# Kernel optimization log

Hardware: AMD Instinct MI355X
Metric: run time of the kernel (lower is better)

## Reference

```python
import jax, jax.numpy as jnp
import numpy as np

NUM_CLASSES = 128
NUM_DOMAINS = 6
FEAT_DIM = 256
B = 524288
MOMENTUM = 0.9
MARGIN = 1.0


def setup_inputs() -> dict:
    key = jax.random.key(0)
    k1, k2, k3, k4, k5, k6 = jax.random.split(key, 6)
    mu_tilde = jax.random.normal(k1, (B, FEAT_DIM), dtype=jnp.float32)
    anchors = jax.random.normal(k2, (NUM_DOMAINS, NUM_CLASSES, FEAT_DIM), dtype=jnp.float32)
    domain_means = jax.random.normal(k3, (NUM_DOMAINS, FEAT_DIM), dtype=jnp.float32)
    domain_vars = jax.random.uniform(k4, (NUM_DOMAINS, FEAT_DIM), dtype=jnp.float32)
    y_true = jax.random.randint(k5, (B,), 0, NUM_CLASSES, dtype=jnp.int32)
    d_true = jax.random.randint(k6, (B,), 0, NUM_DOMAINS, dtype=jnp.int32)
    return {"mu_tilde": mu_tilde, "anchors": anchors, "domain_means": domain_means,
            "domain_vars": domain_vars, "y_true": y_true, "d_true": d_true}


def reference(mu_tilde, anchors, domain_means, domain_vars, y_true, d_true):
    m = MOMENTUM
    one = jnp.asarray(1.0, mu_tilde.dtype)

    # ---- update(): fused per-(domain,class) segment mean + EMA anchor write ----
    seg = d_true.astype(jnp.int32) * NUM_CLASSES + y_true.astype(jnp.int32)
    n_seg = NUM_DOMAINS * NUM_CLASSES
    seg_sum = jax.ops.segment_sum(mu_tilde, seg, num_segments=n_seg)          # (Nd*C, D)
    seg_cnt = jax.ops.segment_sum(jnp.ones((B,), mu_tilde.dtype), seg, num_segments=n_seg)
    seg_mean = seg_sum / jnp.maximum(seg_cnt, one)[:, None]
    has_samples = (seg_cnt > 0).reshape(NUM_DOMAINS, NUM_CLASSES, 1)
    batch_anchor = seg_mean.reshape(NUM_DOMAINS, NUM_CLASSES, FEAT_DIM)
    new_anchors = jnp.where(has_samples, m * anchors + (1.0 - m) * batch_anchor, anchors)

    # ---- update(): per-domain mean/var (unbiased) + EMA ----
    d_sum = jax.ops.segment_sum(mu_tilde, d_true, num_segments=NUM_DOMAINS)
    d_sq = jax.ops.segment_sum(mu_tilde * mu_tilde, d_true, num_segments=NUM_DOMAINS)
    d_cnt = jax.ops.segment_sum(jnp.ones((B,), mu_tilde.dtype), d_true, num_segments=NUM_DOMAINS)
    safe_cnt = jnp.maximum(d_cnt, one)[:, None]
    b_mean = d_sum / safe_cnt
    b_var = (d_sq - safe_cnt * b_mean * b_mean) / jnp.maximum(d_cnt - 1.0, one)[:, None]
    g = (d_cnt > 1)[:, None]
    new_means = jnp.where(g, m * domain_means + (1.0 - m) * b_mean, domain_means)
    new_vars = jnp.where(g, m * domain_vars + (1.0 - m) * b_var, domain_vars)

    # ---- caa_loss() on updated anchors (all anchors initialized) ----
    class_mean = new_anchors.mean(axis=0, keepdims=True)                      # (1, C, D)
    loss_intra = jnp.mean((new_anchors - class_mean) ** 2)                    # avg of per-class MSE
    A_mean = new_anchors.mean(axis=0)                                         # (C, D)
    sq = jnp.sum(A_mean * A_mean, axis=1)
    d2 = sq[:, None] + sq[None, :] - 2.0 * (A_mean @ A_mean.T)
    off_diag = ~jnp.eye(NUM_CLASSES, dtype=bool)
    d2_safe = jnp.where(off_diag, jnp.maximum(d2, 1e-12), 1.0)
    dist = jnp.sqrt(d2_safe)
    loss_inter = jnp.sum(jnp.where(off_diag, jax.nn.relu(MARGIN - dist), 0.0))
    loss_inter = loss_inter / (NUM_CLASSES * (NUM_CLASSES - 1))
    loss_caa = loss_intra + loss_inter

    # ---- stats_align_loss() on updated stats ----
    global_mean = new_means.mean(axis=0)
    global_var = new_vars.mean(axis=0)
    loss_mean = jnp.mean((new_means - global_mean) ** 2)   # sum_d mse / Nd
    loss_var = jnp.mean((new_vars - global_var) ** 2)
    mu_mean = mu_tilde.mean(axis=0)
    mu_var = jnp.mean(mu_tilde * mu_tilde, axis=0) - mu_mean * mu_mean        # biased var
    loss_mu_mean = jnp.mean((mu_mean - global_mean) ** 2)
    loss_mu_var = jnp.mean((mu_var - global_var) ** 2)
    loss_stats = loss_mean + loss_var + loss_mu_mean + loss_mu_var

    return new_anchors, new_means, new_vars, loss_caa + loss_stats
```

## Files before the change

kernel.cpp:

```cpp
#include <hip/hip_runtime.h>

#define B_N   524288
#define FEAT  256
#define NC    128
#define ND    6
#define NSEG  768
#define CAP   1024

#define ZERO_WORDS 3852

__device__ __forceinline__ float block_reduce(float v, float* lds) {
  #pragma unroll
  for (int o = 32; o > 0; o >>= 1) v += __shfl_down(v, o, 64);
  int wid = threadIdx.x >> 6, lane = threadIdx.x & 63;
  if (lane == 0) lds[wid] = v;
  __syncthreads();
  int nw = (blockDim.x + 63) >> 6;
  v = 0.0f;
  if (wid == 0 && lane < nw) v = lds[lane];
  if (wid == 0) {
    #pragma unroll
    for (int o = 4; o > 0; o >>= 1) v += __shfl_down(v, o, 64);
  }
  return v;
}

#define SCHUNK 4096
#define SCAT_BLOCKS (B_N / SCHUNK)
__global__ __launch_bounds__(1024)
void scatter_k(const int* __restrict__ y, const int* __restrict__ dmn,
               int* __restrict__ cursor, int* __restrict__ slots) {
  __shared__ int lcnt[NSEG];
  __shared__ int lbase[NSEG];
  int t = threadIdx.x;
  if (t < NSEG) lcnt[t] = 0;
  __syncthreads();
  int base = blockIdx.x * SCHUNK;
  int segr[4], lposr[4];
  #pragma unroll
  for (int k = 0; k < 4; ++k) {
    int i = base + t + k * 1024;
    int seg = dmn[i] * NC + y[i];
    segr[k] = seg;
    lposr[k] = atomicAdd(&lcnt[seg], 1);
  }
  __syncthreads();
  if (t < NSEG) lbase[t] = atomicAdd(&cursor[t], lcnt[t]);
  __syncthreads();
  #pragma unroll
  for (int k = 0; k < 4; ++k) {
    int i = base + t + k * 1024;
    int p = lbase[segr[k]] + lposr[k];
    if (p < CAP) slots[segr[k] * CAP + p] = i;
  }
}

__global__ __launch_bounds__(512, 1)
void segreduce_k(const float* __restrict__ mu, const int* __restrict__ slots,
                 const int* __restrict__ cursor, float* __restrict__ seg_sum,
                 float* __restrict__ d_sum_acc, float* __restrict__ d_sq_acc,
                 float* __restrict__ d_cnt) {
  int seg = blockIdx.x;
  int cnt = cursor[seg];
  if (cnt > CAP) cnt = CAP;
  int dom = seg >> 7;
  int t  = threadIdx.x;
  int rr = t >> 6;
  int dq = t & 63;
  const int* sl = slots + seg * CAP;
  const size_t doff = (size_t)(dq << 2);

  float ax=0,ay=0,az=0,aw=0, aqx=0,aqy=0,aqz=0,aqw=0;
  float bx=0,by=0,bz=0,bw=0, bqx=0,bqy=0,bqz=0,bqw=0;

  int r = rr;
  int row0 = (r     < cnt) ? sl[r]     : 0;
  int row1 = (r + 8 < cnt) ? sl[r + 8] : 0;
  while (r + 8 < cnt) {
    int n0 = (r + 16 < cnt) ? sl[r + 16] : 0;
    int n1 = (r + 24 < cnt) ? sl[r + 24] : 0;
    const float4 v0 = *reinterpret_cast<const float4*>(mu + (size_t)row0 * FEAT + doff);
    const float4 v1 = *reinterpret_cast<const float4*>(mu + (size_t)row1 * FEAT + doff);
    ax += v0.x; ay += v0.y; az += v0.z; aw += v0.w;
    aqx += v0.x*v0.x; aqy += v0.y*v0.y; aqz += v0.z*v0.z; aqw += v0.w*v0.w;
    bx += v1.x; by += v1.y; bz += v1.z; bw += v1.w;
    bqx += v1.x*v1.x; bqy += v1.y*v1.y; bqz += v1.z*v1.z; bqw += v1.w*v1.w;
    r += 16; row0 = n0; row1 = n1;
  }
  if (r < cnt) {
    const float4 v0 = *reinterpret_cast<const float4*>(mu + (size_t)row0 * FEAT + doff);
    ax += v0.x; ay += v0.y; az += v0.z; aw += v0.w;
    aqx += v0.x*v0.x; aqy += v0.y*v0.y; aqz += v0.z*v0.z; aqw += v0.w*v0.w;
  }
  ax += bx; ay += by; az += bz; aw += bw;
  aqx += bqx; aqy += bqy; aqz += bqz; aqw += bqw;

  __shared__ float4 redS[512];
  __shared__ float4 redQ[512];
  redS[t] = make_float4(ax, ay, az, aw);
  redQ[t] = make_float4(aqx, aqy, aqz, aqw);
  __syncthreads();
  if (rr == 0) {
    float4 s = redS[t], q = redQ[t];
    #pragma unroll
    for (int g = 1; g < 8; ++g) {
      float4 a = redS[t + 64*g]; s.x+=a.x; s.y+=a.y; s.z+=a.z; s.w+=a.w;
      float4 b = redQ[t + 64*g]; q.x+=b.x; q.y+=b.y; q.z+=b.z; q.w+=b.w;
    }
    *reinterpret_cast<float4*>(seg_sum + (size_t)seg * FEAT + (dq << 2)) = s;
    int base = dom * FEAT + (dq << 2);
    atomicAdd(&d_sum_acc[base+0], s.x); atomicAdd(&d_sum_acc[base+1], s.y);
    atomicAdd(&d_sum_acc[base+2], s.z); atomicAdd(&d_sum_acc[base+3], s.w);
    atomicAdd(&d_sq_acc[base+0], q.x);  atomicAdd(&d_sq_acc[base+1], q.y);
    atomicAdd(&d_sq_acc[base+2], q.z);  atomicAdd(&d_sq_acc[base+3], q.w);
  }
  if (t == 0) atomicAdd(&d_cnt[dom], (float)cnt);
}

__global__ void anchors_k(const float* __restrict__ anchors, const float* __restrict__ seg_sum,
                          const int* __restrict__ cursor, float* __restrict__ out_anchors,
                          float* __restrict__ class_mean, float* __restrict__ sqv,
                          float* __restrict__ loss_acc) {
  int c = blockIdx.x;
  int d = threadIdx.x;
  float na[ND];
  float cm = 0.0f;
  #pragma unroll
  for (int dom = 0; dom < ND; ++dom) {
    int segi = dom * NC + c;
    int cnt = cursor[segi];
    float s = seg_sum[(size_t)segi * FEAT + d];
    float mean = s / fmaxf((float)cnt, 1.0f);
    float a = anchors[(size_t)segi * FEAT + d];
    float v = (cnt > 0) ? (0.9f * a + 0.1f * mean) : a;
    out_anchors[(size_t)segi * FEAT + d] = v;
    na[dom] = v;
    cm += v;
  }
  cm /= 6.0f;
  class_mean[c * FEAT + d] = cm;
  float li = 0.0f;
  #pragma unroll
  for (int dom = 0; dom < ND; ++dom) { float e = na[dom] - cm; li += e * e; }

  __shared__ float rbuf[8];
  float r1 = block_reduce(li, rbuf);
  __syncthreads();
  float r2 = block_reduce(cm * cm, rbuf);
  if (threadIdx.x == 0) { atomicAdd(&loss_acc[0], r1); sqv[c] = r2; }
}

__global__ void inter_k(const float* __restrict__ class_mean, const float* __restrict__ sqv,
                        float* __restrict__ loss_acc) {
  int i = blockIdx.x;
  int j = threadIdx.x;
  __shared__ float Ai[FEAT];
  Ai[j]        = class_mean[i * FEAT + j];
  Ai[j + 128]  = class_mean[i * FEAT + 128 + j];
  __syncthreads();
  const float* Aj = class_mean + (size_t)j * FEAT;
  float dot = 0.0f;
  for (int k = 0; k < FEAT; ++k) dot += Ai[k] * Aj[k];
  float contrib = 0.0f;
  if (i != j) {
    float d2 = sqv[i] + sqv[j] - 2.0f * dot;
    d2 = fmaxf(d2, 1e-12f);
    contrib = fmaxf(1.0f - sqrtf(d2), 0.0f);
  }
  __shared__ float rbuf[8];
  float r = block_reduce(contrib, rbuf);
  if (threadIdx.x == 0) atomicAdd(&loss_acc[1], r);
}

__global__ void stats_k(const float* __restrict__ dmeans, const float* __restrict__ dvars,
                        const float* __restrict__ d_sum_acc, const float* __restrict__ d_sq_acc,
                        const float* __restrict__ d_cnt, float* __restrict__ out_means,
                        float* __restrict__ out_vars, float* __restrict__ loss_acc) {
  int d = threadIdx.x;
  float nm[ND], nv[ND];
  float gm = 0.0f, gv = 0.0f, tsum = 0.0f, tsq = 0.0f;
  #pragma unroll
  for (int dom = 0; dom < ND; ++dom) {
    float cf = d_cnt[dom];
    float safe = fmaxf(cf, 1.0f);
    float su = d_sum_acc[dom * FEAT + d];
    float sq = d_sq_acc[dom * FEAT + d];
    tsum += su; tsq += sq;
    float bm = su / safe;
    float bv = (sq - safe * bm * bm) / fmaxf(cf - 1.0f, 1.0f);
    float m0 = dmeans[dom * FEAT + d], v0 = dvars[dom * FEAT + d];
    bool g = cf > 1.0f;
    float m1 = g ? (0.9f * m0 + 0.1f * bm) : m0;
    float v1 = g ? (0.9f * v0 + 0.1f * bv) : v0;
    out_means[dom * FEAT + d] = m1;
    out_vars[dom * FEAT + d]  = v1;
    nm[dom] = m1; nv[dom] = v1; gm += m1; gv += v1;
  }
  gm /= 6.0f; gv /= 6.0f;
  float lm = 0.0f, lv = 0.0f;
  #pragma unroll
  for (int dom = 0; dom < ND; ++dom) {
    float e = nm[dom] - gm; lm += e * e;
    float f = nv[dom] - gv; lv += f * f;
  }
  float mum = tsum * (1.0f / (float)B_N);
  float muv = tsq * (1.0f / (float)B_N) - mum * mum;
  float lmm = (mum - gm) * (mum - gm);
  float lmv = (muv - gv) * (muv - gv);
  float val = (lm + lv) * (1.0f / 1536.0f) + (lmm + lmv) * (1.0f / 256.0f);
  __shared__ float rbuf[8];
  float r = block_reduce(val, rbuf);
  if (threadIdx.x == 0) loss_acc[2] = r;
}

__global__ void final_k(const float* __restrict__ loss_acc, float* __restrict__ out_loss) {
  *out_loss = loss_acc[0] * (1.0f / 196608.0f)
            + loss_acc[1] * (1.0f / 16256.0f)
            + loss_acc[2];
}

extern "C" void kernel_launch(void* const* d_in, const int* in_sizes, int n_in,
                              void* d_out, int out_size, void* d_ws, size_t ws_size,
                              hipStream_t stream) {
  const float* mu      = (const float*)d_in[0];
  const float* anchors = (const float*)d_in[1];
  const float* dmeans  = (const float*)d_in[2];
  const float* dvars   = (const float*)d_in[3];
  const int*   y       = (const int*)d_in[4];
  const int*   dmn     = (const int*)d_in[5];

  float* out = (float*)d_out;
  float* out_anchors = out;
  float* out_means   = out + 196608;
  float* out_vars    = out + 198144;
  float* out_loss    = out + 199680;

  float* wsf       = (float*)d_ws;
  int*   cursor    = (int*)d_ws;
  float* d_cnt     = wsf + 768;
  float* d_sum_acc = wsf + 776;
  float* d_sq_acc  = wsf + 2312;
  float* loss_acc  = wsf + 3848;
  float* seg_sum   = wsf + ZERO_WORDS;
  float* class_mean= seg_sum + NSEG * FEAT;
  float* sqv       = class_mean + NC * FEAT;
  int*   slots     = (int*)(sqv + 128);

  hipMemsetAsync(d_ws, 0, ZERO_WORDS * sizeof(float), stream);
  scatter_k  <<<SCAT_BLOCKS, 1024, 0, stream>>>(y, dmn, cursor, slots);
  segreduce_k<<<NSEG, 512, 0, stream>>>(mu, slots, cursor, seg_sum, d_sum_acc, d_sq_acc, d_cnt);
  anchors_k  <<<NC, 256, 0, stream>>>(anchors, seg_sum, cursor, out_anchors, class_mean, sqv, loss_acc);
  inter_k    <<<NC, 128, 0, stream>>>(class_mean, sqv, loss_acc);
  stats_k    <<<1, 256, 0, stream>>>(dmeans, dvars, d_sum_acc, d_sq_acc, d_cnt, out_means, out_vars, loss_acc);
  final_k    <<<1, 1, 0, stream>>>(loss_acc, out_loss);
}
```

Baseline: 142.1 us.

## Fuse inter, stats and final kernels into one tail kernel; nontemporal gather loads

Merges the inter-class distance, domain stats and final loss kernels into a single launch. The extra stats block runs alongside the class blocks, and a last-block-done counter writes the final loss, which removes two kernel launches. The dot product is split across 256 threads, with each half covering 128 features. segreduce_k switches to nontemporal loads for mu and changes its launch-bounds occupancy hint to 6, which may change register allocation.

```diff
diff --git a/kernel.cpp b/kernel.cpp
--- a/kernel.cpp
+++ b/kernel.cpp
@@ -8,6 +8,8 @@
 #define CAP   1024
 
 #define ZERO_WORDS 3852
+
+typedef float f4v __attribute__((ext_vector_type(4)));
 
 __device__ __forceinline__ float block_reduce(float v, float* lds) {
   #pragma unroll
@@ -55,7 +57,7 @@
   }
 }
 
-__global__ __launch_bounds__(512, 1)
+__global__ __launch_bounds__(512, 6)
 void segreduce_k(const float* __restrict__ mu, const int* __restrict__ slots,
                  const int* __restrict__ cursor, float* __restrict__ seg_sum,
                  float* __restrict__ d_sum_acc, float* __restrict__ d_sq_acc,
@@ -79,8 +81,10 @@
   while (r + 8 < cnt) {
     int n0 = (r + 16 < cnt) ? sl[r + 16] : 0;
     int n1 = (r + 24 < cnt) ? sl[r + 24] : 0;
-    const float4 v0 = *reinterpret_cast<const float4*>(mu + (size_t)row0 * FEAT + doff);
-    const float4 v1 = *reinterpret_cast<const float4*>(mu + (size_t)row1 * FEAT + doff);
+    const f4v v0 = __builtin_nontemporal_load(
+        reinterpret_cast<const f4v*>(mu + (size_t)row0 * FEAT + doff));
+    const f4v v1 = __builtin_nontemporal_load(
+        reinterpret_cast<const f4v*>(mu + (size_t)row1 * FEAT + doff));
     ax += v0.x; ay += v0.y; az += v0.z; aw += v0.w;
     aqx += v0.x*v0.x; aqy += v0.y*v0.y; aqz += v0.z*v0.z; aqw += v0.w*v0.w;
     bx += v1.x; by += v1.y; bz += v1.z; bw += v1.w;
@@ -88,7 +92,8 @@
     r += 16; row0 = n0; row1 = n1;
   }
   if (r < cnt) {
-    const float4 v0 = *reinterpret_cast<const float4*>(mu + (size_t)row0 * FEAT + doff);
+    const f4v v0 = __builtin_nontemporal_load(
+        reinterpret_cast<const f4v*>(mu + (size_t)row0 * FEAT + doff));
     ax += v0.x; ay += v0.y; az += v0.z; aw += v0.w;
     aqx += v0.x*v0.x; aqy += v0.y*v0.y; aqz += v0.z*v0.z; aqw += v0.w*v0.w;
   }
@@ -150,73 +155,87 @@
   if (threadIdx.x == 0) { atomicAdd(&loss_acc[0], r1); sqv[c] = r2; }
 }
 
-__global__ void inter_k(const float* __restrict__ class_mean, const float* __restrict__ sqv,
-                        float* __restrict__ loss_acc) {
-  int i = blockIdx.x;
-  int j = threadIdx.x;
-  __shared__ float Ai[FEAT];
-  Ai[j]        = class_mean[i * FEAT + j];
-  Ai[j + 128]  = class_mean[i * FEAT + 128 + j];
-  __syncthreads();
-  const float* Aj = class_mean + (size_t)j * FEAT;
-  float dot = 0.0f;
-  for (int k = 0; k < FEAT; ++k) dot += Ai[k] * Aj[k];
-  float contrib = 0.0f;
-  if (i != j) {
-    float d2 = sqv[i] + sqv[j] - 2.0f * dot;
-    d2 = fmaxf(d2, 1e-12f);
-    contrib = fmaxf(1.0f - sqrtf(d2), 0.0f);
-  }
+__global__ __launch_bounds__(256)
+void tail_k(const float* __restrict__ class_mean, const float* __restrict__ sqv,
+            const float* __restrict__ dmeans, const float* __restrict__ dvars,
+            const float* __restrict__ d_sum_acc, const float* __restrict__ d_sq_acc,
+            const float* __restrict__ d_cnt, float* __restrict__ out_means,
+            float* __restrict__ out_vars, float* __restrict__ loss_acc,
+            int* __restrict__ done_ctr, float* __restrict__ out_loss) {
+  int b = blockIdx.x;
+  int t = threadIdx.x;
   __shared__ float rbuf[8];
-  float r = block_reduce(contrib, rbuf);
-  if (threadIdx.x == 0) atomicAdd(&loss_acc[1], r);
-}
-
-__global__ void stats_k(const float* __restrict__ dmeans, const float* __restrict__ dvars,
-                        const float* __restrict__ d_sum_acc, const float* __restrict__ d_sq_acc,
-                        const float* __restrict__ d_cnt, float* __restrict__ out_means,
-                        float* __restrict__ out_vars, float* __restrict__ loss_acc) {
-  int d = threadIdx.x;
-  float nm[ND], nv[ND];
-  float gm = 0.0f, gv = 0.0f, tsum = 0.0f, tsq = 0.0f;
-  #pragma unroll
-  for (int dom = 0; dom < ND; ++dom) {
-    float cf = d_cnt[dom];
-    float safe = fmaxf(cf, 1.0f);
-    float su = d_sum_acc[dom * FEAT + d];
-    float sq = d_sq_acc[dom * FEAT + d];
-    tsum += su; tsq += sq;
-    float bm = su / safe;
-    float bv = (sq - safe * bm * bm) / fmaxf(cf - 1.0f, 1.0f);
-    float m0 = dmeans[dom * FEAT + d], v0 = dvars[dom * FEAT + d];
-    bool g = cf > 1.0f;
-    float m1 = g ? (0.9f * m0 + 0.1f * bm) : m0;
-    float v1 = g ? (0.9f * v0 + 0.1f * bv) : v0;
-    out_means[dom * FEAT + d] = m1;
-    out_vars[dom * FEAT + d]  = v1;
-    nm[dom] = m1; nv[dom] = v1; gm += m1; gv += v1;
-  }
-  gm /= 6.0f; gv /= 6.0f;
-  float lm = 0.0f, lv = 0.0f;
-  #pragma unroll
-  for (int dom = 0; dom < ND; ++dom) {
-    float e = nm[dom] - gm; lm += e * e;
-    float f = nv[dom] - gv; lv += f * f;
-  }
-  float mum = tsum * (1.0f / (float)B_N);
-  float muv = tsq * (1.0f / (float)B_N) - mum * mum;
-  float lmm = (mum - gm) * (mum - gm);
-  float lmv = (muv - gv) * (muv - gv);
-  float val = (lm + lv) * (1.0f / 1536.0f) + (lmm + lmv) * (1.0f / 256.0f);
-  __shared__ float rbuf[8];
-  float r = block_reduce(val, rbuf);
-  if (threadIdx.x == 0) loss_acc[2] = r;
-}
-
-__global__ void final_k(const float* __restrict__ loss_acc, float* __restrict__ out_loss) {
-  *out_loss = loss_acc[0] * (1.0f / 196608.0f)
-            + loss_acc[1] * (1.0f / 16256.0f)
-            + loss_acc[2];
+
+  if (b < NC) {
+    __shared__ float Ai[FEAT];
+    __shared__ float dots[256];
+    Ai[t] = class_mean[b * FEAT + t];
+    __syncthreads();
+    int j = t & 127, h = t >> 7;
+    const float* Aj  = class_mean + (size_t)j * FEAT + h * 128;
+    const float* Aih = Ai + h * 128;
+    float dot = 0.0f;
+    #pragma unroll 8
+    for (int k = 0; k < 128; ++k) dot += Aih[k] * Aj[k];
+    dots[t] = dot;
+    __syncthreads();
+    float contrib = 0.0f;
+    if (h == 0 && j != b) {
+      float d2 = sqv[b] + sqv[j] - 2.0f * (dots[j] + dots[j + 128]);
+      d2 = fmaxf(d2, 1e-12f);
+      contrib = fmaxf(1.0f - sqrtf(d2), 0.0f);
+    }
+    float r = block_reduce(contrib, rbuf);
+    if (t == 0) atomicAdd(&loss_acc[1], r);
+  } else {
+    int d = t;
+    float nm[ND], nv[ND];
+    float gm = 0.0f, gv = 0.0f, tsum = 0.0f, tsq = 0.0f;
+    #pragma unroll
+    for (int dom = 0; dom < ND; ++dom) {
+      float cf = d_cnt[dom];
+      float safe = fmaxf(cf, 1.0f);
+      float su = d_sum_acc[dom * FEAT + d];
+      float sq = d_sq_acc[dom * FEAT + d];
+      tsum += su; tsq += sq;
+      float bm = su / safe;
+      float bv = (sq - safe * bm * bm) / fmaxf(cf - 1.0f, 1.0f);
+      float m0 = dmeans[dom * FEAT + d], v0 = dvars[dom * FEAT + d];
+      bool g = cf > 1.0f;
+      float m1 = g ? (0.9f * m0 + 0.1f * bm) : m0;
+      float v1 = g ? (0.9f * v0 + 0.1f * bv) : v0;
+      out_means[dom * FEAT + d] = m1;
+      out_vars[dom * FEAT + d]  = v1;
+      nm[dom] = m1; nv[dom] = v1; gm += m1; gv += v1;
+    }
+    gm /= 6.0f; gv /= 6.0f;
+    float lm = 0.0f, lv = 0.0f;
+    #pragma unroll
+    for (int dom = 0; dom < ND; ++dom) {
+      float e = nm[dom] - gm; lm += e * e;
+      float f = nv[dom] - gv; lv += f * f;
+    }
+    float mum = tsum * (1.0f / (float)B_N);
+    float muv = tsq * (1.0f / (float)B_N) - mum * mum;
+    float lmm = (mum - gm) * (mum - gm);
+    float lmv = (muv - gv) * (muv - gv);
+    float val = (lm + lv) * (1.0f / 1536.0f) + (lmm + lmv) * (1.0f / 256.0f);
+    float r = block_reduce(val, rbuf);
+    if (t == 0) atomicAdd(&loss_acc[2], r);
+  }
+
+  if (t == 0) {
+    __threadfence();
+    int old = atomicAdd(done_ctr, 1);
+    if (old == NC) {
+      float li = atomicAdd(&loss_acc[0], 0.0f);
+      float le = atomicAdd(&loss_acc[1], 0.0f);
+      float ls = atomicAdd(&loss_acc[2], 0.0f);
+      *out_loss = li * (1.0f / 196608.0f)
+                + le * (1.0f / 16256.0f)
+                + ls;
+    }
+  }
 }
 
 extern "C" void kernel_launch(void* const* d_in, const int* in_sizes, int n_in,
@@ -241,6 +260,7 @@
   float* d_sum_acc = wsf + 776;
   float* d_sq_acc  = wsf + 2312;
   float* loss_acc  = wsf + 3848;
+  int*   done_ctr  = (int*)d_ws + 3851;
   float* seg_sum   = wsf + ZERO_WORDS;
   float* class_mean= seg_sum + NSEG * FEAT;
   float* sqv       = class_mean + NC * FEAT;
@@ -250,7 +270,6 @@
   scatter_k  <<<SCAT_BLOCKS, 1024, 0, stream>>>(y, dmn, cursor, slots);
   segreduce_k<<<NSEG, 512, 0, stream>>>(mu, slots, cursor, seg_sum, d_sum_acc, d_sq_acc, d_cnt);
   anchors_k  <<<NC, 256, 0, stream>>>(anchors, seg_sum, cursor, out_anchors, class_mean, sqv, loss_acc);
-  inter_k    <<<NC, 128, 0, stream>>>(class_mean, sqv, loss_acc);
-  stats_k    <<<1, 256, 0, stream>>>(dmeans, dvars, d_sum_acc, d_sq_acc, d_cnt, out_means, out_vars, loss_acc);
-  final_k    <<<1, 1, 0, stream>>>(loss_acc, out_loss);
-}
+  tail_k     <<<NC + 1, 256, 0, stream>>>(class_mean, sqv, dmeans, dvars, d_sum_acc, d_sq_acc,
+                                          d_cnt, out_means, out_vars, loss_acc, done_ctr, out_loss);
+}
```

After: 132.1 us. 1.08x faster.
